# Performance work log

Measured on AMD Instinct MI355X. Metric: run time of the kernel, lower is better.

## Reference

```python
import jax, jax.numpy as jnp
import numpy as np

B, S, D, H = 2, 2048, 1024, 16
DH = D // H  # key_dim = embed_dim // num_heads
NEG = 1e9    # Keras masked-softmax adder magnitude
EPS = 1e-6


def setup_inputs() -> dict:
    key = jax.random.key(0)
    ks = jax.random.split(key, 6)
    sc = 1.0 / np.sqrt(D)
    return {
        "x": jax.random.normal(ks[0], (B, S, D), jnp.float32),
        "Wq": jax.random.normal(ks[1], (D, H, DH), jnp.float32) * sc,
        "bq": jnp.zeros((H, DH), jnp.float32),
        "Wk": jax.random.normal(ks[2], (D, H, DH), jnp.float32) * sc,
        "bk": jnp.zeros((H, DH), jnp.float32),
        "Wv": jax.random.normal(ks[3], (D, H, DH), jnp.float32) * sc,
        "bv": jnp.zeros((H, DH), jnp.float32),
        "Wo": jax.random.normal(ks[4], (H, DH, D), jnp.float32) * (1.0 / np.sqrt(D)),
        "bo": jnp.zeros((D,), jnp.float32),
        "gamma": jnp.ones((D,), jnp.float32),
        "beta": jnp.zeros((D,), jnp.float32),
    }


def reference(x, Wq, bq, Wk, bk, Wv, bv, Wo, bo, gamma, beta):
    # Keras MultiHeadAttention(query=x, value=x), inference (dropouts are identity)
    q = jnp.einsum("bsd,dhk->bshk", x, Wq) + bq  # [B,S,H,DH]
    k = jnp.einsum("bsd,dhk->bshk", x, Wk) + bk
    v = jnp.einsum("bsd,dhk->bshk", x, Wv) + bv

    scores = jnp.einsum("bqhd,bkhd->bhqk", q, k) / jnp.sqrt(jnp.asarray(DH, x.dtype))
    # Source: mask = 1 - band_part(ones, -1, 0) -> ones strictly ABOVE diagonal.
    # Keras attends where mask==1 and adds (1-mask)*(-1e9) elsewhere. Faithful:
    i = jnp.arange(S)[:, None]
    j = jnp.arange(S)[None, :]
    allowed = (j > i).astype(scores.dtype)  # [S,S], strict upper triangle
    scores = scores + (allowed - 1.0) * NEG  # subtract 1e9 where not allowed
    probs = jax.nn.softmax(scores, axis=-1)

    ctx = jnp.einsum("bhqk,bkhd->bqhd", probs, v)  # [B,S,H,DH]
    attn_out = jnp.einsum("bqhd,hdo->bqo", ctx, Wo) + bo  # [B,S,D]

    # residual + LayerNorm(eps=1e-6)
    y = x + attn_out
    mu = jnp.mean(y, axis=-1, keepdims=True)
    var = jnp.mean(jnp.square(y - mu), axis=-1, keepdims=True)
    return (y - mu) * jax.lax.rsqrt(var + EPS) * gamma + beta
```

## Files before the change

### kernel.cpp

```cpp
#include <hip/hip_runtime.h>
#include <hip/hip_bf16.h>

typedef __hip_bfloat16 bf16;
typedef __attribute__((ext_vector_type(8))) short bf16x8;
typedef __attribute__((ext_vector_type(4))) float f32x4;

constexpr int Bc  = 2;
constexpr int Sc  = 2048;
constexpr int Dc  = 1024;
constexpr int Hc  = 16;
constexpr int DHc = 64;
constexpr int BS  = Bc * Sc;
constexpr int NT  = Sc / 64;

__device__ __forceinline__ float bs2f(unsigned short u) {
    union { unsigned int i; float f; } v; v.i = ((unsigned int)u) << 16; return v.f;
}
__device__ __forceinline__ short f2bs(float x) {
    bf16 h = __float2bfloat16(x);
    return *reinterpret_cast<short*>(&h);
}

typedef const __attribute__((address_space(1))) unsigned int* as1_u32p;
typedef __attribute__((address_space(3))) unsigned int* as3_u32p;
__device__ __forceinline__ void gl_lds16(const void* g, void* l) {
    __builtin_amdgcn_global_load_lds((as1_u32p)g, (as3_u32p)l, 16, 0, 0);
}

__global__ __launch_bounds__(256) void cast_x(const float* __restrict__ in,
                                              short* __restrict__ out) {
    const int i = (blockIdx.x * 256 + threadIdx.x) * 4;
    const float4 v = *(const float4*)(in + i);
    ushort4 o;
    o.x = (unsigned short)f2bs(v.x);
    o.y = (unsigned short)f2bs(v.y);
    o.z = (unsigned short)f2bs(v.z);
    o.w = (unsigned short)f2bs(v.w);
    *(ushort4*)(out + i) = o;
}

__global__ __launch_bounds__(256) void transpose_cast(
    const float* __restrict__ w0, const float* __restrict__ w1,
    const float* __restrict__ w2, const float* __restrict__ w3,
    short* __restrict__ outbase)
{
    __shared__ float T[64][65];
    const int z = blockIdx.z;
    const float* in = (z == 0) ? w0 : (z == 1) ? w1 : (z == 2) ? w2 : w3;
    short* out = outbase + (size_t)z * 1024 * 1024;
    const int k0 = blockIdx.x * 64, n0 = blockIdx.y * 64;
    const int t = threadIdx.x;
    #pragma unroll
    for (int it = 0; it < 4; ++it) {
        const int s = it * 256 + t;
        const int r = s >> 4, c = (s & 15) * 4;
        *(float4*)&T[r][c] = *(const float4*)(in + (size_t)(k0 + r) * 1024 + n0 + c);
    }
    __syncthreads();
    #pragma unroll
    for (int it = 0; it < 4; ++it) {
        const int s = it * 256 + t;
        const int rr = s >> 4, cc = (s & 15) * 4;
        ushort4 o;
        o.x = (unsigned short)f2bs(T[cc + 0][rr]);
        o.y = (unsigned short)f2bs(T[cc + 1][rr]);
        o.z = (unsigned short)f2bs(T[cc + 2][rr]);
        o.w = (unsigned short)f2bs(T[cc + 3][rr]);
        *(ushort4*)(out + (size_t)(n0 + rr) * 1024 + k0 + cc) = o;
    }
}

__global__ __launch_bounds__(256, 3) void gemm_bt(
    const short* __restrict__ A, const short* __restrict__ BTbase,
    const float* __restrict__ b0, const float* __restrict__ b1,
    const float* __restrict__ b2, short* __restrict__ Cbase)
{
    __shared__ __align__(16) short As[128 * 64];
    __shared__ __align__(16) short Bs[128 * 64];

    const int z = blockIdx.z;
    const short* BT = BTbase + (size_t)z * 1024 * 1024;
    const float* bias = (z == 0) ? b0 : (z == 1) ? b1 : b2;
    short* C = Cbase + (size_t)z * BS * Dc;

    const int t = threadIdx.x;
    const int lane = t & 63, w = t >> 6;
    const int quad = lane >> 4, l16 = lane & 15;
    const int wm = (w & 1) * 64, wn = (w >> 1) * 64;
    const int row0 = blockIdx.y * 128;
    const int col0 = blockIdx.x * 128;
    const int sw = l16 & 7;

    f32x4 acc[4][4] = {};

    for (int kt = 0; kt < 1024; kt += 64) {
        __syncthreads();
        #pragma unroll
        for (int i = 0; i < 4; ++i) {
            const int f = i * 256 + t;
            const int r = f >> 3;
            const int g = (f & 7) ^ (r & 7);
            short* lb = &As[(i * 256 + w * 64) * 8];
            gl_lds16(A + (size_t)(row0 + r) * 1024 + kt + g * 8, lb);
            short* lb2 = &Bs[(i * 256 + w * 64) * 8];
            gl_lds16(BT + (size_t)(col0 + r) * 1024 + kt + g * 8, lb2);
        }
        __syncthreads();
        #pragma unroll
        for (int ks = 0; ks < 2; ++ks) {
            bf16x8 av[4], bv[4];
            #pragma unroll
            for (int mt = 0; mt < 4; ++mt) {
                const int r = wm + mt * 16 + l16;
                av[mt] = *(const bf16x8*)&As[r * 64 + ((ks * 4 + quad) ^ sw) * 8];
            }
            #pragma unroll
            for (int nt = 0; nt < 4; ++nt) {
                const int r = wn + nt * 16 + l16;
                bv[nt] = *(const bf16x8*)&Bs[r * 64 + ((ks * 4 + quad) ^ sw) * 8];
            }
            #pragma unroll
            for (int mt = 0; mt < 4; ++mt)
                #pragma unroll
                for (int nt = 0; nt < 4; ++nt)
                    acc[mt][nt] = __builtin_amdgcn_mfma_f32_16x16x32_bf16(
                        av[mt], bv[nt], acc[mt][nt], 0, 0, 0);
        }
    }

    float bvv[4];
    #pragma unroll
    for (int nt = 0; nt < 4; ++nt) bvv[nt] = bias[col0 + wn + nt * 16 + l16];
    #pragma unroll
    for (int mt = 0; mt < 4; ++mt)
        #pragma unroll
        for (int reg = 0; reg < 4; ++reg) {
            const size_t row = row0 + wm + mt * 16 + quad * 4 + reg;
            #pragma unroll
            for (int nt = 0; nt < 4; ++nt) {
                const int col = col0 + wn + nt * 16 + l16;
                C[row * 1024 + col] = f2bs(acc[mt][nt][reg] + bvv[nt]);
            }
        }
}


template<bool DIAG>
__device__ __forceinline__ void qtile_step(
    const bf16x8 (&qf)[2],
    const short (&Ks)[64][72], const short (&VsT)[64][72],
    short (&Psw)[16][72],
    const int k0, const int row_base,
    const int quad, const int l16,
    float (&l)[4], f32x4 (&O)[4])
{
    bf16x8 kf[2][4];
    #pragma unroll
    for (int ks = 0; ks < 2; ++ks)
        #pragma unroll
        for (int nt = 0; nt < 4; ++nt)
            kf[ks][nt] = *(const bf16x8*)&Ks[nt * 16 + l16][ks * 32 + quad * 8];

    f32x4 S[4] = {};
    #pragma unroll
    for (int ks = 0; ks < 2; ++ks)
        #pragma unroll
        for (int nt = 0; nt < 4; ++nt)
            S[nt] = __builtin_amdgcn_mfma_f32_16x16x32_bf16(qf[ks], kf[ks][nt], S[nt], 0, 0, 0);

    #pragma unroll
    for (int nt = 0; nt < 4; ++nt) {
        #pragma unroll
        for (int reg = 0; reg < 4; ++reg) {
            float s = fminf(S[nt][reg] * 0.18033688f, 115.4f);
            if (DIAG) {
                const int col = k0 + nt * 16 + l16;
                const int row = row_base + quad * 4 + reg;
                s = (col > row) ? s : -126.0f;
            }
            const float p = exp2f(s);
            S[nt][reg] = p;
            l[reg] += p;
        }
    }

    #pragma unroll
    for (int reg = 0; reg < 4; ++reg) {
        const __hip_bfloat162 lo = __float22bfloat162_rn(make_float2(S[0][reg], S[1][reg]));
        const __hip_bfloat162 hi = __float22bfloat162_rn(make_float2(S[2][reg], S[3][reg]));
        uint2 u;
        u.x = *reinterpret_cast<const unsigned int*>(&lo);
        u.y = *reinterpret_cast<const unsigned int*>(&hi);
        *(uint2*)&Psw[quad * 4 + reg][l16 * 4] = u;
    }

    #pragma unroll
    for (int ks = 0; ks < 2; ++ks) {
        const bf16x8 pf = *(const bf16x8*)&Psw[l16][ks * 32 + quad * 8];
        #pragma unroll
        for (int nt = 0; nt < 4; ++nt) {
            const bf16x8 vf = *(const bf16x8*)&VsT[nt * 16 + l16][ks * 32 + quad * 8];
            O[nt] = __builtin_amdgcn_mfma_f32_16x16x32_bf16(pf, vf, O[nt], 0, 0, 0);
        }
    }
}

__global__ __launch_bounds__(256, 3) void attn_mfma(
    const short* __restrict__ Qg, const short* __restrict__ Kg,
    const short* __restrict__ Vg, short* __restrict__ CTX)
{
    __shared__ __align__(16) short Ks [2][64][72];
    __shared__ __align__(16) short VsT[2][64][72];
    __shared__ __align__(16) short Ps[4][16][72];

    const int tid  = threadIdx.x;
    const int lane = tid & 63, w = tid >> 6;
    const int quad = lane >> 4, l16 = lane & 15;
    const int p  = blockIdx.x;
    const int h  = blockIdx.y;
    const int b  = blockIdx.z;
    const size_t rb = (size_t)b * Sc;
    const int cb = h * DHc;

    const int skey = tid & 63, sseg = (tid >> 6) * 8;
    const int pkey = ((skey & 15) << 2) | (skey >> 4);

    #pragma unroll 1
    for (int ph = 0; ph < 2; ++ph) {
        const int myq = ph ? (NT - 1 - p) : p;
        const int t0  = myq;
        const int q0  = myq * 64;

        bf16x8 qf[2];
        {
            const short* qp = Qg + (rb + q0 + w * 16 + l16) * (size_t)Dc + cb + quad * 8;
            qf[0] = *(const bf16x8*)(qp);
            qf[1] = *(const bf16x8*)(qp + 32);
        }
        float l[4] = {};
        f32x4 O[4] = {};

        if (ph) __syncthreads();

        {
            const int buf = t0 & 1;
            const size_t g = (rb + t0 * 64 + skey) * (size_t)Dc + cb + sseg;
            const bf16x8 k0v = *(const bf16x8*)(Kg + g);
            const bf16x8 k1v = *(const bf16x8*)(Kg + g + 32);
            const bf16x8 v0v = *(const bf16x8*)(Vg + g);
            const bf16x8 v1v = *(const bf16x8*)(Vg + g + 32);
            *(bf16x8*)&Ks[buf][skey][sseg]      = k0v;
            *(bf16x8*)&Ks[buf][skey][sseg + 32] = k1v;
            #pragma unroll
            for (int e = 0; e < 8; ++e) {
                VsT[buf][sseg + e][pkey]      = v0v[e];
                VsT[buf][sseg + 32 + e][pkey] = v1v[e];
            }
        }
        __syncthreads();

        for (int t = t0; t < NT; ++t) {
            const int cur = t & 1;
            const bool havenext = (t + 1 < NT);
            bf16x8 pk0, pk1, pv0, pv1;
            if (havenext) {
                const size_t g = (rb + (t + 1) * 64 + skey) * (size_t)Dc + cb + sseg;
                pk0 = *(const bf16x8*)(Kg + g);
                pk1 = *(const bf16x8*)(Kg + g + 32);
                pv0 = *(const bf16x8*)(Vg + g);
                pv1 = *(const bf16x8*)(Vg + g + 32);
            }

            if (t == t0)
                qtile_step<true >(qf, Ks[cur], VsT[cur], Ps[w],
                                  t * 64, q0 + w * 16, quad, l16, l, O);
            else
                qtile_step<false>(qf, Ks[cur], VsT[cur], Ps[w],
                                  t * 64, q0 + w * 16, quad, l16, l, O);

            if (havenext) {
                const int nb = cur ^ 1;
                *(bf16x8*)&Ks[nb][skey][sseg]      = pk0;
                *(bf16x8*)&Ks[nb][skey][sseg + 32] = pk1;
                #pragma unroll
                for (int e = 0; e < 8; ++e) {
                    VsT[nb][sseg + e][pkey]      = pv0[e];
                    VsT[nb][sseg + 32 + e][pkey] = pv1[e];
                }
                __syncthreads();
            }
        }

        #pragma unroll
        for (int off = 1; off < 16; off <<= 1)
            #pragma unroll
            for (int reg = 0; reg < 4; ++reg)
                l[reg] += __shfl_xor(l[reg], off, 64);
        #pragma unroll
        for (int reg = 0; reg < 4; ++reg) l[reg] = 1.0f / l[reg];
        #pragma unroll
        for (int nt = 0; nt < 4; ++nt)
            #pragma unroll
            for (int reg = 0; reg < 4; ++reg) {
                const size_t row = rb + q0 + w * 16 + quad * 4 + reg;
                CTX[row * Dc + cb + nt * 16 + l16] = f2bs(O[nt][reg] * l[reg]);
            }
    }
}

__global__ __launch_bounds__(256) void vmean(const short* __restrict__ V,
                                             short* __restrict__ CTX)
{
    const int h = blockIdx.x, b = blockIdx.y;
    const int t = threadIdx.x;
    const int dh = t & 63, ck = t >> 6;
    float s = 0.f;
    const short* vp = V + ((size_t)b * Sc + ck * 512) * Dc + h * DHc + dh;
    for (int j = 0; j < 512; ++j) s += bs2f(vp[(size_t)j * Dc]);
    __shared__ float red[4][64];
    red[ck][dh] = s;
    __syncthreads();
    if (ck == 0) {
        const float tot = (red[0][dh] + red[1][dh] + red[2][dh] + red[3][dh]) * (1.f / Sc);
        CTX[((size_t)b * Sc + Sc - 1) * Dc + h * DHc + dh] = f2bs(tot);
    }
}

__global__ __launch_bounds__(256, 4) void resid_ln(
    const float* __restrict__ X, const short* __restrict__ AO,
    const float* __restrict__ gamma, const float* __restrict__ beta,
    float* __restrict__ out)
{
    const int r = blockIdx.x;
    const int t = threadIdx.x;
    const size_t base = (size_t)r * Dc + t * 4;

    const float4 x4 = *(const float4*)(X + base);
    const ushort4 a4 = *(const ushort4*)(AO + base);
    float y[4];
    y[0] = x4.x + bs2f(a4.x);
    y[1] = x4.y + bs2f(a4.y);
    y[2] = x4.z + bs2f(a4.z);
    y[3] = x4.w + bs2f(a4.w);

    float s  = y[0] + y[1] + y[2] + y[3];
    float s2 = y[0]*y[0] + y[1]*y[1] + y[2]*y[2] + y[3]*y[3];
    #pragma unroll
    for (int off = 1; off < 64; off <<= 1) {
        s  += __shfl_xor(s,  off, 64);
        s2 += __shfl_xor(s2, off, 64);
    }
    __shared__ float red[8];
    const int w = t >> 6;
    if ((t & 63) == 0) { red[w] = s; red[4 + w] = s2; }
    __syncthreads();
    s  = red[0] + red[1] + red[2] + red[3];
    s2 = red[4] + red[5] + red[6] + red[7];

    const float mu   = s * (1.0f / Dc);
    const float rstd = rsqrtf(s2 * (1.0f / Dc) - mu * mu + 1e-6f);

    const float4 g4 = *(const float4*)(gamma + t * 4);
    const float4 b4 = *(const float4*)(beta  + t * 4);
    float4 o;
    o.x = (y[0] - mu) * rstd * g4.x + b4.x;
    o.y = (y[1] - mu) * rstd * g4.y + b4.y;
    o.z = (y[2] - mu) * rstd * g4.z + b4.z;
    o.w = (y[3] - mu) * rstd * g4.w + b4.w;
    *(float4*)(out + base) = o;
}

extern "C" void kernel_launch(void* const* d_in, const int* in_sizes, int n_in,
                              void* d_out, int out_size, void* d_ws, size_t ws_size,
                              hipStream_t stream)
{
    (void)in_sizes; (void)n_in; (void)out_size; (void)ws_size;
    const float* x     = (const float*)d_in[0];
    const float* Wq    = (const float*)d_in[1];
    const float* bq    = (const float*)d_in[2];
    const float* Wk    = (const float*)d_in[3];
    const float* bk    = (const float*)d_in[4];
    const float* Wv    = (const float*)d_in[5];
    const float* bv    = (const float*)d_in[6];
    const float* Wo    = (const float*)d_in[7];
    const float* bo    = (const float*)d_in[8];
    const float* gamma = (const float*)d_in[9];
    const float* beta  = (const float*)d_in[10];
    float* out = (float*)d_out;

    const size_t matN = (size_t)BS * Dc;
    const size_t wN   = (size_t)Dc * Dc;
    short* xb = (short*)d_ws;
    short* WT = xb + matN;
    short* Qb = WT + 4 * wN;
    short* Kb = Qb + matN;
    short* Vb = Kb + matN;
    short* Cx = Vb + matN;
    short* AO = Qb;

    cast_x<<<matN / 1024, 256, 0, stream>>>(x, xb);

    dim3 gt(16, 16, 4);
    transpose_cast<<<gt, 256, 0, stream>>>(Wq, Wk, Wv, Wo, WT);

    dim3 gq(Dc / 128, BS / 128, 3);
    gemm_bt<<<gq, 256, 0, stream>>>(xb, WT, bq, bk, bv, Qb);

    dim3 ga(16, Hc, Bc);
    attn_mfma<<<ga, 256, 0, stream>>>(Qb, Kb, Vb, Cx);

    dim3 gv(Hc, Bc);
    vmean<<<gv, 256, 0, stream>>>(Vb, Cx);

    dim3 go(Dc / 128, BS / 128, 1);
    gemm_bt<<<go, 256, 0, stream>>>(Cx, WT + 3 * wN, bo, bo, bo, AO);

    resid_ln<<<BS, 256, 0, stream>>>(x, AO, gamma, beta, out);
}
```

Before: 221.6 us.

## Load K fragments directly from global into registers and split attention blocks per q-tile

K tiles are no longer staged in shared memory. Each wave loads its MFMA K fragments straight from global memory into registers and prefetches the next tile while the current scores are computed. The paired two-phase q-tile loop is split so each block handles one q-tile, which doubles the grid, and launch bounds rise to 4 blocks per CU. This removes the LDS writes and reads for K and adds parallelism, at the cost of redundant global K loads across the four waves, more register pressure, and per-block load imbalance from the causal work.

```diff
diff --git a/kernel.cpp b/kernel.cpp
--- a/kernel.cpp
+++ b/kernel.cpp
@@ -146,28 +146,13 @@
 
 
 template<bool DIAG>
-__device__ __forceinline__ void qtile_step(
-    const bf16x8 (&qf)[2],
-    const short (&Ks)[64][72], const short (&VsT)[64][72],
-    short (&Psw)[16][72],
+__device__ __forceinline__ void sm_pv(
+    f32x4 (&S)[4],
+    const short (&VsT)[64][72], short (&Psw)[16][72],
     const int k0, const int row_base,
     const int quad, const int l16,
     float (&l)[4], f32x4 (&O)[4])
 {
-    bf16x8 kf[2][4];
-    #pragma unroll
-    for (int ks = 0; ks < 2; ++ks)
-        #pragma unroll
-        for (int nt = 0; nt < 4; ++nt)
-            kf[ks][nt] = *(const bf16x8*)&Ks[nt * 16 + l16][ks * 32 + quad * 8];
-
-    f32x4 S[4] = {};
-    #pragma unroll
-    for (int ks = 0; ks < 2; ++ks)
-        #pragma unroll
-        for (int nt = 0; nt < 4; ++nt)
-            S[nt] = __builtin_amdgcn_mfma_f32_16x16x32_bf16(qf[ks], kf[ks][nt], S[nt], 0, 0, 0);
-
     #pragma unroll
     for (int nt = 0; nt < 4; ++nt) {
         #pragma unroll
@@ -205,107 +190,117 @@
     }
 }
 
-__global__ __launch_bounds__(256, 3) void attn_mfma(
+__global__ __launch_bounds__(256, 4) void attn_mfma(
     const short* __restrict__ Qg, const short* __restrict__ Kg,
     const short* __restrict__ Vg, short* __restrict__ CTX)
 {
-    __shared__ __align__(16) short Ks [2][64][72];
     __shared__ __align__(16) short VsT[2][64][72];
     __shared__ __align__(16) short Ps[4][16][72];
 
     const int tid  = threadIdx.x;
     const int lane = tid & 63, w = tid >> 6;
     const int quad = lane >> 4, l16 = lane & 15;
-    const int p  = blockIdx.x;
+    const int x  = blockIdx.x;
     const int h  = blockIdx.y;
     const int b  = blockIdx.z;
     const size_t rb = (size_t)b * Sc;
     const int cb = h * DHc;
 
+    const int myq = (x & 1) ? (NT - 1 - (x >> 1)) : (x >> 1);
+    const int t0  = myq;
+    const int q0  = myq * 64;
+
+    bf16x8 qf[2];
+    {
+        const short* qp = Qg + (rb + q0 + w * 16 + l16) * (size_t)Dc + cb + quad * 8;
+        qf[0] = *(const bf16x8*)(qp);
+        qf[1] = *(const bf16x8*)(qp + 32);
+    }
+    float l[4] = {};
+    f32x4 O[4] = {};
+
     const int skey = tid & 63, sseg = (tid >> 6) * 8;
     const int pkey = ((skey & 15) << 2) | (skey >> 4);
 
-    #pragma unroll 1
-    for (int ph = 0; ph < 2; ++ph) {
-        const int myq = ph ? (NT - 1 - p) : p;
-        const int t0  = myq;
-        const int q0  = myq * 64;
-
-        bf16x8 qf[2];
-        {
-            const short* qp = Qg + (rb + q0 + w * 16 + l16) * (size_t)Dc + cb + quad * 8;
-            qf[0] = *(const bf16x8*)(qp);
-            qf[1] = *(const bf16x8*)(qp + 32);
-        }
-        float l[4] = {};
-        f32x4 O[4] = {};
-
-        if (ph) __syncthreads();
-
-        {
-            const int buf = t0 & 1;
-            const size_t g = (rb + t0 * 64 + skey) * (size_t)Dc + cb + sseg;
-            const bf16x8 k0v = *(const bf16x8*)(Kg + g);
-            const bf16x8 k1v = *(const bf16x8*)(Kg + g + 32);
-            const bf16x8 v0v = *(const bf16x8*)(Vg + g);
-            const bf16x8 v1v = *(const bf16x8*)(Vg + g + 32);
-            *(bf16x8*)&Ks[buf][skey][sseg]      = k0v;
-            *(bf16x8*)&Ks[buf][skey][sseg + 32] = k1v;
+    bf16x8 kf[2][4];
+    {
+        const short* kp = Kg + (rb + t0 * 64 + l16) * (size_t)Dc + cb + quad * 8;
+        #pragma unroll
+        for (int ks = 0; ks < 2; ++ks)
+            #pragma unroll
+            for (int nt = 0; nt < 4; ++nt)
+                kf[ks][nt] = *(const bf16x8*)(kp + (size_t)nt * 16 * Dc + ks * 32);
+    }
+
+    {
+        const int buf = t0 & 1;
+        const size_t g = (rb + t0 * 64 + skey) * (size_t)Dc + cb + sseg;
+        const bf16x8 v0v = *(const bf16x8*)(Vg + g);
+        const bf16x8 v1v = *(const bf16x8*)(Vg + g + 32);
+        #pragma unroll
+        for (int e = 0; e < 8; ++e) {
+            VsT[buf][sseg + e][pkey]      = v0v[e];
+            VsT[buf][sseg + 32 + e][pkey] = v1v[e];
+        }
+    }
+    __syncthreads();
+
+    for (int t = t0; t < NT; ++t) {
+        const int cur = t & 1;
+        const bool havenext = (t + 1 < NT);
+        bf16x8 pv0, pv1;
+        if (havenext) {
+            const size_t g = (rb + (t + 1) * 64 + skey) * (size_t)Dc + cb + sseg;
+            pv0 = *(const bf16x8*)(Vg + g);
+            pv1 = *(const bf16x8*)(Vg + g + 32);
+        }
+
+        f32x4 S[4] = {};
+        #pragma unroll
+        for (int ks = 0; ks < 2; ++ks)
+            #pragma unroll
+            for (int nt = 0; nt < 4; ++nt)
+                S[nt] = __builtin_amdgcn_mfma_f32_16x16x32_bf16(qf[ks], kf[ks][nt], S[nt], 0, 0, 0);
+
+        if (havenext) {
+            const short* kp = Kg + (rb + (t + 1) * 64 + l16) * (size_t)Dc + cb + quad * 8;
+            #pragma unroll
+            for (int ks = 0; ks < 2; ++ks)
+                #pragma unroll
+                for (int nt = 0; nt < 4; ++nt)
+                    kf[ks][nt] = *(const bf16x8*)(kp + (size_t)nt * 16 * Dc + ks * 32);
+        }
+
+        if (t == t0)
+            sm_pv<true >(S, VsT[cur], Ps[w], t * 64, q0 + w * 16, quad, l16, l, O);
+        else
+            sm_pv<false>(S, VsT[cur], Ps[w], t * 64, q0 + w * 16, quad, l16, l, O);
+
+        if (havenext) {
+            const int nb = cur ^ 1;
             #pragma unroll
             for (int e = 0; e < 8; ++e) {
-                VsT[buf][sseg + e][pkey]      = v0v[e];
-                VsT[buf][sseg + 32 + e][pkey] = v1v[e];
+                VsT[nb][sseg + e][pkey]      = pv0[e];
+                VsT[nb][sseg + 32 + e][pkey] = pv1[e];
             }
-        }
-        __syncthreads();
-
-        for (int t = t0; t < NT; ++t) {
-            const int cur = t & 1;
-            const bool havenext = (t + 1 < NT);
-            bf16x8 pk0, pk1, pv0, pv1;
-            if (havenext) {
-                const size_t g = (rb + (t + 1) * 64 + skey) * (size_t)Dc + cb + sseg;
-                pk0 = *(const bf16x8*)(Kg + g);
-                pk1 = *(const bf16x8*)(Kg + g + 32);
-                pv0 = *(const bf16x8*)(Vg + g);
-                pv1 = *(const bf16x8*)(Vg + g + 32);
-            }
-
-            if (t == t0)
-                qtile_step<true >(qf, Ks[cur], VsT[cur], Ps[w],
-                                  t * 64, q0 + w * 16, quad, l16, l, O);
-            else
-                qtile_step<false>(qf, Ks[cur], VsT[cur], Ps[w],
-                                  t * 64, q0 + w * 16, quad, l16, l, O);
-
-            if (havenext) {
-                const int nb = cur ^ 1;
-                *(bf16x8*)&Ks[nb][skey][sseg]      = pk0;
-                *(bf16x8*)&Ks[nb][skey][sseg + 32] = pk1;
-                #pragma unroll
-                for (int e = 0; e < 8; ++e) {
-                    VsT[nb][sseg + e][pkey]      = pv0[e];
-                    VsT[nb][sseg + 32 + e][pkey] = pv1[e];
-                }
-                __syncthreads();
-            }
-        }
-
-        #pragma unroll
-        for (int off = 1; off < 16; off <<= 1)
-            #pragma unroll
-            for (int reg = 0; reg < 4; ++reg)
-                l[reg] += __shfl_xor(l[reg], off, 64);
-        #pragma unroll
-        for (int reg = 0; reg < 4; ++reg) l[reg] = 1.0f / l[reg];
-        #pragma unroll
-        for (int nt = 0; nt < 4; ++nt)
-            #pragma unroll
-            for (int reg = 0; reg < 4; ++reg) {
-                const size_t row = rb + q0 + w * 16 + quad * 4 + reg;
-                CTX[row * Dc + cb + nt * 16 + l16] = f2bs(O[nt][reg] * l[reg]);
-            }
-    }
+            __syncthreads();
+        }
+    }
+
+    #pragma unroll
+    for (int off = 1; off < 16; off <<= 1)
+        #pragma unroll
+        for (int reg = 0; reg < 4; ++reg)
+            l[reg] += __shfl_xor(l[reg], off, 64);
+    #pragma unroll
+    for (int reg = 0; reg < 4; ++reg) l[reg] = 1.0f / l[reg];
+    #pragma unroll
+    for (int nt = 0; nt < 4; ++nt)
+        #pragma unroll
+        for (int reg = 0; reg < 4; ++reg) {
+            const size_t row = rb + q0 + w * 16 + quad * 4 + reg;
+            CTX[row * Dc + cb + nt * 16 + l16] = f2bs(O[nt][reg] * l[reg]);
+        }
 }
 
 __global__ __launch_bounds__(256) void vmean(const short* __restrict__ V,
@@ -406,7 +401,7 @@
     dim3 gq(Dc / 128, BS / 128, 3);
     gemm_bt<<<gq, 256, 0, stream>>>(xb, WT, bq, bk, bv, Qb);
 
-    dim3 ga(16, Hc, Bc);
+    dim3 ga(32, Hc, Bc);
     attn_mfma<<<ga, 256, 0, stream>>>(Qb, Kb, Vb, Cx);
 
     dim3 gv(Hc, Bc);
```

Result: slower. 317.3 us (+43.2%).

## Split attention KV tiles across two wave groups per block and merge partial outputs

Applied to the files above, without the earlier changes.

The attention kernel now uses 512 threads per block, with two groups of four waves each handling alternating 64-key tiles for the same query tiles. Each group keeps its own buffer, and the partial numerators and denominators are merged through shared memory at the end. Block indices are also remapped to spread heads and batches across XCDs. This raises per-CU parallelism and halves the serial key-loop length, at the cost of extra barriers, a shared-memory merge step, and losing the double-buffered prefetch overlap within a group.

```diff
diff --git a/kernel.cpp b/kernel.cpp
--- a/kernel.cpp
+++ b/kernel.cpp
@@ -205,87 +205,101 @@
     }
 }
 
-__global__ __launch_bounds__(256, 3) void attn_mfma(
+__global__ __launch_bounds__(512, 4) void attn_mfma(
     const short* __restrict__ Qg, const short* __restrict__ Kg,
     const short* __restrict__ Vg, short* __restrict__ CTX)
 {
     __shared__ __align__(16) short Ks [2][64][72];
     __shared__ __align__(16) short VsT[2][64][72];
-    __shared__ __align__(16) short Ps[4][16][72];
+    __shared__ __align__(16) short Ps[8][16][72];
+    float* omrg = (float*)&Ps[0][0][0];
+    float* lmrg = omrg + 64 * 65;
 
     const int tid  = threadIdx.x;
     const int lane = tid & 63, w = tid >> 6;
     const int quad = lane >> 4, l16 = lane & 15;
-    const int p  = blockIdx.x;
-    const int h  = blockIdx.y;
-    const int b  = blockIdx.z;
+    const int g  = w >> 2;
+    const int wq = w & 3;
+
+    const int f  = blockIdx.x + 16 * blockIdx.y + 256 * blockIdx.z;
+    const int r_ = (f & 7) * 64 + (f >> 3);
+    const int p  = r_ & 15;
+    const int h  = (r_ >> 4) & 15;
+    const int b  = r_ >> 8;
     const size_t rb = (size_t)b * Sc;
     const int cb = h * DHc;
 
-    const int skey = tid & 63, sseg = (tid >> 6) * 8;
-    const int pkey = ((skey & 15) << 2) | (skey >> 4);
+    const int tid8  = tid & 255;
+    const int skey  = tid8 >> 2;
+    const int sslot = (tid8 & 3) * 16;
+    const int pkey  = ((skey & 15) << 2) | (skey >> 4);
 
     #pragma unroll 1
     for (int ph = 0; ph < 2; ++ph) {
         const int myq = ph ? (NT - 1 - p) : p;
-        const int t0  = myq;
+        const int n   = NT - myq;
+        const int c0  = (n + 1) >> 1;
+        const int c1  = n >> 1;
+        const int cg  = g ? c1 : c0;
+        const int R   = c0;
         const int q0  = myq * 64;
 
         bf16x8 qf[2];
         {
-            const short* qp = Qg + (rb + q0 + w * 16 + l16) * (size_t)Dc + cb + quad * 8;
+            const short* qp = Qg + (rb + q0 + wq * 16 + l16) * (size_t)Dc + cb + quad * 8;
             qf[0] = *(const bf16x8*)(qp);
             qf[1] = *(const bf16x8*)(qp + 32);
         }
         float l[4] = {};
         f32x4 O[4] = {};
 
-        if (ph) __syncthreads();
-
-        {
-            const int buf = t0 & 1;
-            const size_t g = (rb + t0 * 64 + skey) * (size_t)Dc + cb + sseg;
-            const bf16x8 k0v = *(const bf16x8*)(Kg + g);
-            const bf16x8 k1v = *(const bf16x8*)(Kg + g + 32);
-            const bf16x8 v0v = *(const bf16x8*)(Vg + g);
-            const bf16x8 v1v = *(const bf16x8*)(Vg + g + 32);
-            *(bf16x8*)&Ks[buf][skey][sseg]      = k0v;
-            *(bf16x8*)&Ks[buf][skey][sseg + 32] = k1v;
+        if (cg > 0) {
+            const size_t ga = (rb + (myq + g) * 64 + skey) * (size_t)Dc + cb + sslot;
+            const bf16x8 k0v = *(const bf16x8*)(Kg + ga);
+            const bf16x8 k1v = *(const bf16x8*)(Kg + ga + 8);
+            const bf16x8 v0v = *(const bf16x8*)(Vg + ga);
+            const bf16x8 v1v = *(const bf16x8*)(Vg + ga + 8);
+            *(bf16x8*)&Ks[g][skey][sslot]     = k0v;
+            *(bf16x8*)&Ks[g][skey][sslot + 8] = k1v;
             #pragma unroll
             for (int e = 0; e < 8; ++e) {
-                VsT[buf][sseg + e][pkey]      = v0v[e];
-                VsT[buf][sseg + 32 + e][pkey] = v1v[e];
+                VsT[g][sslot + e][pkey]     = v0v[e];
+                VsT[g][sslot + 8 + e][pkey] = v1v[e];
             }
         }
         __syncthreads();
 
-        for (int t = t0; t < NT; ++t) {
-            const int cur = t & 1;
-            const bool havenext = (t + 1 < NT);
+        for (int i = 0; i < R; ++i) {
+            const bool pre = (i + 1 < cg);
             bf16x8 pk0, pk1, pv0, pv1;
-            if (havenext) {
-                const size_t g = (rb + (t + 1) * 64 + skey) * (size_t)Dc + cb + sseg;
-                pk0 = *(const bf16x8*)(Kg + g);
-                pk1 = *(const bf16x8*)(Kg + g + 32);
-                pv0 = *(const bf16x8*)(Vg + g);
-                pv1 = *(const bf16x8*)(Vg + g + 32);
-            }
-
-            if (t == t0)
-                qtile_step<true >(qf, Ks[cur], VsT[cur], Ps[w],
-                                  t * 64, q0 + w * 16, quad, l16, l, O);
-            else
-                qtile_step<false>(qf, Ks[cur], VsT[cur], Ps[w],
-                                  t * 64, q0 + w * 16, quad, l16, l, O);
-
-            if (havenext) {
-                const int nb = cur ^ 1;
-                *(bf16x8*)&Ks[nb][skey][sseg]      = pk0;
-                *(bf16x8*)&Ks[nb][skey][sseg + 32] = pk1;
-                #pragma unroll
-                for (int e = 0; e < 8; ++e) {
-                    VsT[nb][sseg + e][pkey]      = pv0[e];
-                    VsT[nb][sseg + 32 + e][pkey] = pv1[e];
+            if (pre) {
+                const size_t ga = (rb + (myq + g + 2 * (i + 1)) * 64 + skey) * (size_t)Dc + cb + sslot;
+                pk0 = *(const bf16x8*)(Kg + ga);
+                pk1 = *(const bf16x8*)(Kg + ga + 8);
+                pv0 = *(const bf16x8*)(Vg + ga);
+                pv1 = *(const bf16x8*)(Vg + ga + 8);
+            }
+
+            if (i < cg) {
+                const int t = myq + g + 2 * i;
+                if (i == 0 && g == 0)
+                    qtile_step<true >(qf, Ks[0], VsT[0], Ps[w],
+                                      t * 64, q0 + wq * 16, quad, l16, l, O);
+                else
+                    qtile_step<false>(qf, Ks[g], VsT[g], Ps[w],
+                                      t * 64, q0 + wq * 16, quad, l16, l, O);
+            }
+
+            if (i + 1 < R) {
+                __syncthreads();
+                if (pre) {
+                    *(bf16x8*)&Ks[g][skey][sslot]     = pk0;
+                    *(bf16x8*)&Ks[g][skey][sslot + 8] = pk1;
+                    #pragma unroll
+                    for (int e = 0; e < 8; ++e) {
+                        VsT[g][sslot + e][pkey]     = pv0[e];
+                        VsT[g][sslot + 8 + e][pkey] = pv1[e];
+                    }
                 }
                 __syncthreads();
             }
@@ -296,15 +310,32 @@
             #pragma unroll
             for (int reg = 0; reg < 4; ++reg)
                 l[reg] += __shfl_xor(l[reg], off, 64);
-        #pragma unroll
-        for (int reg = 0; reg < 4; ++reg) l[reg] = 1.0f / l[reg];
-        #pragma unroll
-        for (int nt = 0; nt < 4; ++nt)
+
+        __syncthreads();
+        if (g == 1) {
+            #pragma unroll
+            for (int nt = 0; nt < 4; ++nt)
+                #pragma unroll
+                for (int reg = 0; reg < 4; ++reg)
+                    omrg[(wq * 16 + quad * 4 + reg) * 65 + nt * 16 + l16] = O[nt][reg];
+            if (l16 == 0)
+                #pragma unroll
+                for (int reg = 0; reg < 4; ++reg)
+                    lmrg[wq * 16 + quad * 4 + reg] = l[reg];
+        }
+        __syncthreads();
+        if (g == 0) {
             #pragma unroll
             for (int reg = 0; reg < 4; ++reg) {
-                const size_t row = rb + q0 + w * 16 + quad * 4 + reg;
-                CTX[row * Dc + cb + nt * 16 + l16] = f2bs(O[nt][reg] * l[reg]);
-            }
+                const int row = wq * 16 + quad * 4 + reg;
+                const float inv = 1.0f / (l[reg] + lmrg[row]);
+                #pragma unroll
+                for (int nt = 0; nt < 4; ++nt) {
+                    const float o = O[nt][reg] + omrg[row * 65 + nt * 16 + l16];
+                    CTX[(rb + q0 + row) * Dc + cb + nt * 16 + l16] = f2bs(o * inv);
+                }
+            }
+        }
     }
 }
 
@@ -406,8 +437,8 @@
     dim3 gq(Dc / 128, BS / 128, 3);
     gemm_bt<<<gq, 256, 0, stream>>>(xb, WT, bq, bk, bv, Qb);
 
-    dim3 ga(16, Hc, Bc);
-    attn_mfma<<<ga, 256, 0, stream>>>(Qb, Kb, Vb, Cx);
+    dim3 ga(16, 16, 2);
+    attn_mfma<<<ga, 512, 0, stream>>>(Qb, Kb, Vb, Cx);
 
     dim3 gv(Hc, Bc);
     vmean<<<gv, 256, 0, stream>>>(Vb, Cx);
```

After: 219.1 us. About the same (-1.1%).
